# Kernel tuning notes

Hardware: AMD Instinct MI355X
Metric: run time of the kernel (lower is better)

Reference implementation:

```python
import jax, jax.numpy as jnp
import numpy as np

N_BUS = 2048


def setup_inputs() -> dict:
    key = jax.random.key(0)
    ks = jax.random.split(key, 16)
    n_x, n_rbf, n_bus, batch = 4096, 1024, N_BUS, 8192
    s = lambda fan_in: 1.0 / np.sqrt(fan_in)
    return {
        "x": jax.random.normal(ks[0], (batch, n_x), dtype=jnp.float32),
        "W_h": jax.random.uniform(ks[1], (n_rbf, n_x), jnp.float32, -s(n_x), s(n_x)),
        "b_h": jax.random.uniform(ks[2], (n_rbf,), jnp.float32, -s(n_x), s(n_x)),
        "W_h2": jax.random.uniform(ks[3], (n_rbf, n_rbf), jnp.float32, -s(n_rbf), s(n_rbf)),
        "b_h2": jax.random.uniform(ks[4], (n_rbf,), jnp.float32, -s(n_rbf), s(n_rbf)),
        "W_y": jax.random.uniform(ks[5], (2 * n_bus, n_rbf), jnp.float32, -s(n_rbf), s(n_rbf)),
        "b_y": jax.random.uniform(ks[6], (2 * n_bus,), jnp.float32, -s(n_rbf), s(n_rbf)),
        "G": jax.random.uniform(ks[7], (n_bus, n_bus), dtype=jnp.float32),
        "Bm": jax.random.uniform(ks[8], (n_bus, n_bus), dtype=jnp.float32),
        "bias_p": jnp.zeros((1, n_bus), jnp.float32),
        "bias_q": jnp.zeros((1, n_bus), jnp.float32),
        "W_p": jax.random.uniform(ks[9], (n_bus, n_bus), jnp.float32, -s(n_bus), s(n_bus)),
        "b_p": jax.random.uniform(ks[10], (n_bus,), jnp.float32, -s(n_bus), s(n_bus)),
        "W_q": jax.random.uniform(ks[11], (n_bus, n_bus), jnp.float32, -s(n_bus), s(n_bus)),
        "b_q": jax.random.uniform(ks[12], (n_bus,), jnp.float32, -s(n_bus), s(n_bus)),
    }


def reference(x, W_h, b_h, W_h2, b_h2, W_y, b_y, G, Bm, bias_p, bias_q, W_p, b_p, W_q, b_q):
    n_bus = N_BUS
    # encoder (intended math: ReLU activations)
    h1 = jax.nn.relu(x @ W_h.T + b_h)
    h2 = jax.nn.relu(h1 @ W_h2.T + b_h2)
    uw = h2 @ W_y.T + b_y                     # [B, 2*n_bus]
    u, w = uw[:, :n_bus], uw[:, n_bus:]
    # decoder: algebraically identical to summing the masked outer products over dim 2:
    # p_i = sum_k (u_i u_k + w_i w_k) G_ik + (w_i u_k - u_i w_k) B_ik
    #     = u_i (G u)_i + w_i (G w)_i + w_i (B u)_i - u_i (B w)_i
    Gu = u @ G.T
    Gw = w @ G.T
    Bu = u @ Bm.T
    Bw = w @ Bm.T
    p = u * Gu + w * Gw + w * Bu - u * Bw + bias_p
    q = w * Gu - u * Gw - u * Bu - w * Bw + bias_q
    p = p @ W_p.T + b_p
    q = q @ W_q.T + b_q
    return (uw, p, q)
```

## Files before the change

kernel.cpp:

```cpp
#include <hip/hip_runtime.h>

typedef __bf16 bf16;
typedef __bf16 bf16x8 __attribute__((ext_vector_type(8)));
typedef __bf16 bf16x4 __attribute__((ext_vector_type(4)));
typedef float  f32x4  __attribute__((ext_vector_type(4)));

__device__ __forceinline__ void async_load16(const void* g, void* l) {
    __builtin_amdgcn_global_load_lds(
        (const __attribute__((address_space(1))) void*)g,
        (__attribute__((address_space(3))) void*)l,
        16, 0, 0);
}

__global__ __launch_bounds__(256) void cast_f32_bf16(
        const float* __restrict__ s, bf16* __restrict__ d, int n) {
    int i = (blockIdx.x * 256 + threadIdx.x) * 8;
    if (i >= n) return;
    f32x4 v0 = *(const f32x4*)(s + i);
    f32x4 v1 = *(const f32x4*)(s + i + 4);
    bf16x8 o;
    o[0] = (bf16)v0[0]; o[1] = (bf16)v0[1]; o[2] = (bf16)v0[2]; o[3] = (bf16)v0[3];
    o[4] = (bf16)v1[0]; o[5] = (bf16)v1[1]; o[6] = (bf16)v1[2]; o[7] = (bf16)v1[3];
    *(bf16x8*)(d + i) = o;
}

__global__ __launch_bounds__(256) void fill_f32(float* p, float v, int n) {
    int i = blockIdx.x * 256 + threadIdx.x;
    if (i < n) p[i] = v;
}

template<int RELU, int WF32, int WBF16>
__global__ __launch_bounds__(256, 2) void gemm_bt(
        const bf16* __restrict__ A, int lda,
        const bf16* __restrict__ B, int ldb,
        const float* __restrict__ bias,
        float* __restrict__ Cf, int ldcf,
        bf16* __restrict__ Cb, int ldcb,
        int M, int N, int K) {
    (void)M; (void)N;
    __shared__ __attribute__((aligned(16))) bf16 lA[128 * 32];
    __shared__ __attribute__((aligned(16))) bf16 lB[128 * 32];

    const int t = threadIdx.x;
    const int w = t >> 6, lane = t & 63;
    const int wm = w >> 1, wn = w & 1;
    const int m0 = blockIdx.y * 128, n0 = blockIdx.x * 128;
    const int lane15 = lane & 15, quad = lane >> 4;

    f32x4 acc[4][4] = {};

    const int srow = lane >> 2;
    const int scol = (lane & 3) * 8;
    const int c0 = 2 * w, c1 = 2 * w + 1;
    const bf16* gA0 = A + (size_t)(m0 + c0 * 16 + srow) * lda + scol;
    const bf16* gA1 = A + (size_t)(m0 + c1 * 16 + srow) * lda + scol;
    const bf16* gB0 = B + (size_t)(n0 + c0 * 16 + srow) * ldb + scol;
    const bf16* gB1 = B + (size_t)(n0 + c1 * 16 + srow) * ldb + scol;
    bf16* lA0 = &lA[c0 * 512];
    bf16* lA1 = &lA[c1 * 512];
    bf16* lB0 = &lB[c0 * 512];
    bf16* lB1 = &lB[c1 * 512];

    const bf16* fA = &lA[(wm * 64 + lane15) * 32 + quad * 8];
    const bf16* fB = &lB[(wn * 64 + lane15) * 32 + quad * 8];

    for (int k0 = 0; k0 < K; k0 += 32) {
        async_load16(gA0, lA0);
        async_load16(gA1, lA1);
        async_load16(gB0, lB0);
        async_load16(gB1, lB1);
        gA0 += 32; gA1 += 32; gB0 += 32; gB1 += 32;
        __syncthreads();
        bf16x8 a[4], b[4];
#pragma unroll
        for (int i = 0; i < 4; i++) a[i] = *(const bf16x8*)(fA + i * 16 * 32);
#pragma unroll
        for (int j = 0; j < 4; j++) b[j] = *(const bf16x8*)(fB + j * 16 * 32);
#pragma unroll
        for (int i = 0; i < 4; i++)
#pragma unroll
            for (int j = 0; j < 4; j++)
                acc[i][j] = __builtin_amdgcn_mfma_f32_16x16x32_bf16(a[i], b[j], acc[i][j], 0, 0, 0);
        __syncthreads();
    }

#pragma unroll
    for (int i = 0; i < 4; i++) {
        int row = m0 + wm * 64 + i * 16 + quad * 4;
#pragma unroll
        for (int j = 0; j < 4; j++) {
            int col = n0 + wn * 64 + j * 16 + lane15;
            float bv = bias ? bias[col] : 0.0f;
#pragma unroll
            for (int r = 0; r < 4; r++) {
                float v = acc[i][j][r] + bv;
                if (RELU) v = v > 0.0f ? v : 0.0f;
                if (WF32)  Cf[(size_t)(row + r) * ldcf + col] = v;
                if (WBF16) Cb[(size_t)(row + r) * ldcb + col] = (bf16)v;
            }
        }
    }
}

__global__ __launch_bounds__(256) void combine_pq(
        const float* __restrict__ uw,
        const bf16* __restrict__ Gu, const bf16* __restrict__ Gw,
        const bf16* __restrict__ Bu, const bf16* __restrict__ Bw,
        const float* __restrict__ bias_p, const float* __restrict__ bias_q,
        bf16* __restrict__ pp, bf16* __restrict__ qp) {
    int idx = (blockIdx.x * 256 + threadIdx.x) * 4;
    int row = idx >> 11;
    int col = idx & 2047;
    const float* up = uw + (size_t)row * 4096 + col;
    f32x4 u4 = *(const f32x4*)up;
    f32x4 w4 = *(const f32x4*)(up + 2048);
    bf16x4 gu4 = *(const bf16x4*)(Gu + idx);
    bf16x4 gw4 = *(const bf16x4*)(Gw + idx);
    bf16x4 bu4 = *(const bf16x4*)(Bu + idx);
    bf16x4 bw4 = *(const bf16x4*)(Bw + idx);
    bf16x4 po, qo;
#pragma unroll
    for (int r = 0; r < 4; r++) {
        float u = u4[r], w = w4[r];
        float gu = (float)gu4[r], gw = (float)gw4[r];
        float bu = (float)bu4[r], bw = (float)bw4[r];
        float p = u * gu + w * gw + w * bu - u * bw + bias_p[col + r];
        float q = w * gu - u * gw - u * bu - w * bw + bias_q[col + r];
        po[r] = (bf16)p;
        qo[r] = (bf16)q;
    }
    *(bf16x4*)(pp + idx) = po;
    *(bf16x4*)(qp + idx) = qo;
}

extern "C" void kernel_launch(void* const* d_in, const int* in_sizes, int n_in,
                              void* d_out, int out_size, void* d_ws, size_t ws_size,
                              hipStream_t stream) {
    (void)in_sizes; (void)n_in;
    const int BT = 8192, NX = 4096, NR = 1024, NB = 2048;

    const float* x      = (const float*)d_in[0];
    const float* W_h    = (const float*)d_in[1];
    const float* b_h    = (const float*)d_in[2];
    const float* W_h2   = (const float*)d_in[3];
    const float* b_h2   = (const float*)d_in[4];
    const float* W_y    = (const float*)d_in[5];
    const float* b_y    = (const float*)d_in[6];
    const float* G      = (const float*)d_in[7];
    const float* Bm     = (const float*)d_in[8];
    const float* bias_p = (const float*)d_in[9];
    const float* bias_q = (const float*)d_in[10];
    const float* W_p    = (const float*)d_in[11];
    const float* b_p    = (const float*)d_in[12];
    const float* W_q    = (const float*)d_in[13];
    const float* b_q    = (const float*)d_in[14];
    float* out = (float*)d_out;

    const size_t NEED = 287309824ull;
    if (ws_size < NEED) {
        fill_f32<<<dim3((out_size + 255) / 256), dim3(256), 0, stream>>>(
            out, (float)(ws_size >> 20), out_size);
        return;
    }
    char* ws = (char*)d_ws;
    bf16* xb   = (bf16*)(ws + 0);
    bf16* Gu   = (bf16*)(ws + 0);
    bf16* Gw   = (bf16*)(ws + 33554432);
    bf16* uwb  = (bf16*)(ws + 67108864);
    bf16* qp   = (bf16*)(ws + 67108864);
    bf16* Bu   = (bf16*)(ws + 134217728);
    bf16* Bw   = (bf16*)(ws + 167772160);
    bf16* h1   = (bf16*)(ws + 201326592);
    bf16* pp   = (bf16*)(ws + 201326592);
    bf16* h2   = (bf16*)(ws + 218103808);
    bf16* whb  = (bf16*)(ws + 234881024);
    bf16* wh2b = (bf16*)(ws + 243269632);
    bf16* wyb  = (bf16*)(ws + 245366784);
    bf16* gb   = (bf16*)(ws + 253755392);
    bf16* bmb  = (bf16*)(ws + 262144000);
    bf16* wpb  = (bf16*)(ws + 270532608);
    bf16* wqb  = (bf16*)(ws + 278921216);

    dim3 blk(256);
    auto cast = [&](const float* s, bf16* d, int n) {
        cast_f32_bf16<<<dim3((n / 8 + 255) / 256), blk, 0, stream>>>(s, d, n);
    };
    cast(x,    xb,   BT * NX);
    cast(W_h,  whb,  NR * NX);
    cast(W_h2, wh2b, NR * NR);
    cast(W_y,  wyb,  NX * NR);
    cast(G,    gb,   NB * NB);
    cast(Bm,   bmb,  NB * NB);
    cast(W_p,  wpb,  NB * NB);
    cast(W_q,  wqb,  NB * NB);

    gemm_bt<1, 0, 1><<<dim3(NR / 128, BT / 128), blk, 0, stream>>>(
        xb, NX, whb, NX, b_h, nullptr, 0, h1, NR, BT, NR, NX);
    gemm_bt<1, 0, 1><<<dim3(NR / 128, BT / 128), blk, 0, stream>>>(
        h1, NR, wh2b, NR, b_h2, nullptr, 0, h2, NR, BT, NR, NR);
    gemm_bt<0, 1, 1><<<dim3(NX / 128, BT / 128), blk, 0, stream>>>(
        h2, NR, wyb, NR, b_y, out, NX, uwb, NX, BT, NX, NR);
    gemm_bt<0, 0, 1><<<dim3(NB / 128, BT / 128), blk, 0, stream>>>(
        uwb,      NX, gb,  NB, nullptr, nullptr, 0, Gu, NB, BT, NB, NB);
    gemm_bt<0, 0, 1><<<dim3(NB / 128, BT / 128), blk, 0, stream>>>(
        uwb + NB, NX, gb,  NB, nullptr, nullptr, 0, Gw, NB, BT, NB, NB);
    gemm_bt<0, 0, 1><<<dim3(NB / 128, BT / 128), blk, 0, stream>>>(
        uwb,      NX, bmb, NB, nullptr, nullptr, 0, Bu, NB, BT, NB, NB);
    gemm_bt<0, 0, 1><<<dim3(NB / 128, BT / 128), blk, 0, stream>>>(
        uwb + NB, NX, bmb, NB, nullptr, nullptr, 0, Bw, NB, BT, NB, NB);
    combine_pq<<<dim3(BT * NB / 4 / 256), blk, 0, stream>>>(
        out, Gu, Gw, Bu, Bw, bias_p, bias_q, pp, qp);
    gemm_bt<0, 1, 0><<<dim3(NB / 128, BT / 128), blk, 0, stream>>>(
        pp, NB, wpb, NB, b_p, out + (size_t)BT * NX, NB, nullptr, 0, BT, NB, NB);
    gemm_bt<0, 1, 0><<<dim3(NB / 128, BT / 128), blk, 0, stream>>>(
        qp, NB, wqb, NB, b_q, out + (size_t)BT * NX + (size_t)BT * NB, NB, nullptr, 0, BT, NB, NB);
}
```

Measured before the change: 1.242 ms.

## Merge G and B decoder GEMMs into wide GEMMs and read bf16 uw in combine

Stacks G and Bm into one contiguous bf16 weight so each of u and w needs a single 4096-wide GEMM instead of two 2048-wide ones, halving decoder GEMM launches and reusing each A tile across both matrices. The combine kernel now reads the bf16 copy of uw instead of the fp32 output, cutting its memory traffic. Launch bounds raise the min-blocks hint to 3, which may force register spills. The workspace grows and buffers are relaid out.

```diff
diff --git a/kernel.cpp b/kernel.cpp
--- a/kernel.cpp
+++ b/kernel.cpp
@@ -30,7 +30,7 @@
 }
 
 template<int RELU, int WF32, int WBF16>
-__global__ __launch_bounds__(256, 2) void gemm_bt(
+__global__ __launch_bounds__(256, 3) void gemm_bt(
         const bf16* __restrict__ A, int lda,
         const bf16* __restrict__ B, int ldb,
         const float* __restrict__ bias,
@@ -103,25 +103,24 @@
 }
 
 __global__ __launch_bounds__(256) void combine_pq(
-        const float* __restrict__ uw,
-        const bf16* __restrict__ Gu, const bf16* __restrict__ Gw,
-        const bf16* __restrict__ Bu, const bf16* __restrict__ Bw,
+        const bf16* __restrict__ uwb,
+        const bf16* __restrict__ GBu, const bf16* __restrict__ GBw,
         const float* __restrict__ bias_p, const float* __restrict__ bias_q,
         bf16* __restrict__ pp, bf16* __restrict__ qp) {
     int idx = (blockIdx.x * 256 + threadIdx.x) * 4;
     int row = idx >> 11;
     int col = idx & 2047;
-    const float* up = uw + (size_t)row * 4096 + col;
-    f32x4 u4 = *(const f32x4*)up;
-    f32x4 w4 = *(const f32x4*)(up + 2048);
-    bf16x4 gu4 = *(const bf16x4*)(Gu + idx);
-    bf16x4 gw4 = *(const bf16x4*)(Gw + idx);
-    bf16x4 bu4 = *(const bf16x4*)(Bu + idx);
-    bf16x4 bw4 = *(const bf16x4*)(Bw + idx);
+    size_t base = (size_t)row * 4096 + col;
+    bf16x4 u4  = *(const bf16x4*)(uwb + base);
+    bf16x4 w4  = *(const bf16x4*)(uwb + base + 2048);
+    bf16x4 gu4 = *(const bf16x4*)(GBu + base);
+    bf16x4 bu4 = *(const bf16x4*)(GBu + base + 2048);
+    bf16x4 gw4 = *(const bf16x4*)(GBw + base);
+    bf16x4 bw4 = *(const bf16x4*)(GBw + base + 2048);
     bf16x4 po, qo;
 #pragma unroll
     for (int r = 0; r < 4; r++) {
-        float u = u4[r], w = w4[r];
+        float u = (float)u4[r], w = (float)w4[r];
         float gu = (float)gu4[r], gw = (float)gw4[r];
         float bu = (float)bu4[r], bw = (float)bw4[r];
         float p = u * gu + w * gw + w * bu - u * bw + bias_p[col + r];
@@ -156,7 +155,7 @@
     const float* b_q    = (const float*)d_in[14];
     float* out = (float*)d_out;
 
-    const size_t NEED = 287309824ull;
+    const size_t NEED = 320864256ull;
     if (ws_size < NEED) {
         fill_f32<<<dim3((out_size + 255) / 256), dim3(256), 0, stream>>>(
             out, (float)(ws_size >> 20), out_size);
@@ -164,22 +163,19 @@
     }
     char* ws = (char*)d_ws;
     bf16* xb   = (bf16*)(ws + 0);
-    bf16* Gu   = (bf16*)(ws + 0);
-    bf16* Gw   = (bf16*)(ws + 33554432);
+    bf16* GBu  = (bf16*)(ws + 0);
     bf16* uwb  = (bf16*)(ws + 67108864);
-    bf16* qp   = (bf16*)(ws + 67108864);
-    bf16* Bu   = (bf16*)(ws + 134217728);
-    bf16* Bw   = (bf16*)(ws + 167772160);
+    bf16* GBw  = (bf16*)(ws + 134217728);
     bf16* h1   = (bf16*)(ws + 201326592);
     bf16* pp   = (bf16*)(ws + 201326592);
     bf16* h2   = (bf16*)(ws + 218103808);
-    bf16* whb  = (bf16*)(ws + 234881024);
-    bf16* wh2b = (bf16*)(ws + 243269632);
-    bf16* wyb  = (bf16*)(ws + 245366784);
-    bf16* gb   = (bf16*)(ws + 253755392);
-    bf16* bmb  = (bf16*)(ws + 262144000);
-    bf16* wpb  = (bf16*)(ws + 270532608);
-    bf16* wqb  = (bf16*)(ws + 278921216);
+    bf16* qp   = (bf16*)(ws + 234881024);
+    bf16* whb  = (bf16*)(ws + 268435456);
+    bf16* wh2b = (bf16*)(ws + 276824064);
+    bf16* wyb  = (bf16*)(ws + 278921216);
+    bf16* gbm  = (bf16*)(ws + 287309824);
+    bf16* wpb  = (bf16*)(ws + 304087040);
+    bf16* wqb  = (bf16*)(ws + 312475648);
 
     dim3 blk(256);
     auto cast = [&](const float* s, bf16* d, int n) {
@@ -189,8 +185,8 @@
     cast(W_h,  whb,  NR * NX);
     cast(W_h2, wh2b, NR * NR);
     cast(W_y,  wyb,  NX * NR);
-    cast(G,    gb,   NB * NB);
-    cast(Bm,   bmb,  NB * NB);
+    cast(G,    gbm,            NB * NB);
+    cast(Bm,   gbm + (size_t)NB * NB, NB * NB);
     cast(W_p,  wpb,  NB * NB);
     cast(W_q,  wqb,  NB * NB);
 
@@ -200,16 +196,12 @@
         h1, NR, wh2b, NR, b_h2, nullptr, 0, h2, NR, BT, NR, NR);
     gemm_bt<0, 1, 1><<<dim3(NX / 128, BT / 128), blk, 0, stream>>>(
         h2, NR, wyb, NR, b_y, out, NX, uwb, NX, BT, NX, NR);
-    gemm_bt<0, 0, 1><<<dim3(NB / 128, BT / 128), blk, 0, stream>>>(
-        uwb,      NX, gb,  NB, nullptr, nullptr, 0, Gu, NB, BT, NB, NB);
-    gemm_bt<0, 0, 1><<<dim3(NB / 128, BT / 128), blk, 0, stream>>>(
-        uwb + NB, NX, gb,  NB, nullptr, nullptr, 0, Gw, NB, BT, NB, NB);
-    gemm_bt<0, 0, 1><<<dim3(NB / 128, BT / 128), blk, 0, stream>>>(
-        uwb,      NX, bmb, NB, nullptr, nullptr, 0, Bu, NB, BT, NB, NB);
-    gemm_bt<0, 0, 1><<<dim3(NB / 128, BT / 128), blk, 0, stream>>>(
-        uwb + NB, NX, bmb, NB, nullptr, nullptr, 0, Bw, NB, BT, NB, NB);
+    gemm_bt<0, 0, 1><<<dim3(NX / 128, BT / 128), blk, 0, stream>>>(
+        uwb,      NX, gbm, NB, nullptr, nullptr, 0, GBu, NX, BT, NX, NB);
+    gemm_bt<0, 0, 1><<<dim3(NX / 128, BT / 128), blk, 0, stream>>>(
+        uwb + NB, NX, gbm, NB, nullptr, nullptr, 0, GBw, NX, BT, NX, NB);
     combine_pq<<<dim3(BT * NB / 4 / 256), blk, 0, stream>>>(
-        out, Gu, Gw, Bu, Bw, bias_p, bias_q, pp, qp);
+        uwb, GBu, GBw, bias_p, bias_q, pp, qp);
     gemm_bt<0, 1, 0><<<dim3(NB / 128, BT / 128), blk, 0, stream>>>(
         pp, NB, wpb, NB, b_p, out + (size_t)BT * NX, NB, nullptr, 0, BT, NB, NB);
     gemm_bt<0, 1, 0><<<dim3(NB / 128, BT / 128), blk, 0, stream>>>(
```

New measurement: 1.205 ms. 1.03x faster.
